# Kernel tuning notes

Measured on AMD Instinct MI355X. Metric: run time of the kernel, lower is better.

Reference implementation:

```python
import jax, jax.numpy as jnp
import numpy as np

B, T, D, H, L = 32, 1024, 512, 512, 2
FORGET_BIAS = 1.0


def setup_inputs() -> dict:
    key = jax.random.key(0)
    k_x, k_len, k_wf, k_wb = jax.random.split(key, 4)
    inputs = jax.random.normal(k_x, (B, T, D), dtype=jnp.float32)
    lengths = jax.random.randint(k_len, (B,), 1, T + 1, dtype=jnp.int32)
    scale = 1.0 / np.sqrt(D + H)
    # Stacked per-layer weights; layer input dim == H == D so shapes match.
    Wf = jax.random.normal(k_wf, (L, D + H, 4 * H), dtype=jnp.float32) * scale
    Wb = jax.random.normal(k_wb, (L, D + H, 4 * H), dtype=jnp.float32) * scale
    bf = jnp.zeros((L, 4 * H), dtype=jnp.float32)
    bb = jnp.zeros((L, 4 * H), dtype=jnp.float32)
    return {"inputs": inputs, "lengths": lengths, "Wf": Wf, "bf": bf, "Wb": Wb, "bb": bb}


def _reverse_sequence(x_bt, lengths):
    # TF reverse_sequence semantics: reverse the first `len` steps, keep the tail.
    t = jnp.arange(x_bt.shape[1])[None, :]                      # [1,T]
    ln = lengths[:, None]                                       # [B,1]
    idx = jnp.where(t < ln, ln - 1 - t, t)                      # [B,T]
    return jnp.take_along_axis(x_bt, idx[:, :, None], axis=1)


def _lstm_layer(xs_tb, W, b, lengths):
    # xs_tb: [T,B,In]; tf.contrib LSTMCell gate order: i, j(candidate), f, o.
    Bdim = xs_tb.shape[1]
    h0 = jnp.zeros((Bdim, H), xs_tb.dtype)
    c0 = jnp.zeros((Bdim, H), xs_tb.dtype)
    ts = jnp.arange(xs_tb.shape[0])

    def step(carry, inp):
        h, c = carry
        x, t = inp
        z = jnp.concatenate([x, h], axis=-1) @ W + b             # [B,4H]
        i, j, f, o = jnp.split(z, 4, axis=-1)
        c_new = jax.nn.sigmoid(f + FORGET_BIAS) * c + jax.nn.sigmoid(i) * jnp.tanh(j)
        h_new = jax.nn.sigmoid(o) * jnp.tanh(c_new)
        m = (t < lengths)[:, None]
        # dynamic_rnn: freeze state past length, emit zeros past length
        c_keep = jnp.where(m, c_new, c)
        h_keep = jnp.where(m, h_new, h)
        y = jnp.where(m, h_new, 0.0)
        return (h_keep, c_keep), y

    (hT, cT), ys = jax.lax.scan(step, (h0, c0), (xs_tb, ts))
    return ys, hT, cT


def reference(inputs, lengths, Wf, bf, Wb, bb):
    # Forward-direction stacked LSTM
    h = jnp.transpose(inputs, (1, 0, 2))                         # [T,B,D]
    for l in range(L):
        h, _, _ = _lstm_layer(h, Wf[l], bf[l], lengths)
    out_f = jnp.transpose(h, (1, 0, 2))                          # [B,T,H]

    # Backward direction: reverse by length, run stack, reverse back
    xr = _reverse_sequence(inputs, lengths)
    h = jnp.transpose(xr, (1, 0, 2))
    for l in range(L):
        h, _, _ = _lstm_layer(h, Wb[l], bb[l], lengths)
    out_b = _reverse_sequence(jnp.transpose(h, (1, 0, 2)), lengths)

    return jnp.concatenate([out_f, out_b], axis=2)               # [B,T,2H]
```

## Files before the change

kernel.cpp:

```cpp
#include <hip/hip_runtime.h>
#include <stdint.h>


#define B_ 32
#define T_ 1024
#define H_ 512

typedef __attribute__((ext_vector_type(8))) short bf16x8;
typedef __attribute__((ext_vector_type(4))) float f32x4;
typedef __attribute__((ext_vector_type(4))) unsigned int u32x4;
typedef unsigned long long ull;

#define FLAG_OFF  0
#define H_OFF     4096
#define H_GRP_U64 (2 * 8192)
#define R_OFF     (H_OFF + 4 * 2 * 65536)
#define R_DIR_U64 (8 * 4096)
#define WS_BYTES  (R_OFF + 2 * 8 * 32768)

#define BLO_OFF   0
#define BHI_OFF   65536
#define ZB0_OFF   131072
#define ZB1_OFF   (ZB0_OFF + 4224)
#define LDS_BYTES (ZB1_OFF + 4224)

#define LOADA(p)     __hip_atomic_load((p), __ATOMIC_RELAXED, __HIP_MEMORY_SCOPE_AGENT)
#define STOREA(p, v) __hip_atomic_store((p), (v), __ATOMIC_RELAXED, __HIP_MEMORY_SCOPE_AGENT)

__device__ __forceinline__ float sigm(float x) { return 1.f / (1.f + __expf(-x)); }
__device__ __forceinline__ unsigned short bf16_rtn(float f) {
  unsigned u = __builtin_bit_cast(unsigned, f);
  unsigned r = u + 0x7FFFu + ((u >> 16) & 1u);
  return (unsigned short)(r >> 16);
}
__device__ __forceinline__ float bf16f(unsigned short h) {
  return __builtin_bit_cast(float, (unsigned)h << 16);
}
__device__ __forceinline__ void split_f32(float f, unsigned short& hi, unsigned short& lo) {
  hi = bf16_rtn(f); lo = bf16_rtn(f - bf16f(hi));
}
__device__ __forceinline__ unsigned packhi2(float fa, float fb) {
  return __builtin_amdgcn_perm(__builtin_bit_cast(unsigned, fb),
                               __builtin_bit_cast(unsigned, fa), 0x07060302u);
}
__device__ __forceinline__ float hipart(float f) {
  return __builtin_bit_cast(float, __builtin_bit_cast(unsigned, f) & 0xFFFF0000u);
}
__device__ __forceinline__ unsigned hiPair(unsigned w0, unsigned w1) {
  return __builtin_amdgcn_perm(w1, w0, 0x07060302u);
}
__device__ __forceinline__ unsigned loPair(unsigned w0, unsigned w1) {
  return __builtin_amdgcn_perm(w1, w0, 0x05040100u);
}

#define MFMA(ACC, Af, Bf) ACC = __builtin_amdgcn_mfma_f32_16x16x32_bf16((Af), (Bf), (ACC), 0, 0, 0)

__global__ __launch_bounds__(256, 1)
void bilstm_v5(const float* __restrict__ inp, const int* __restrict__ lens,
               const float* __restrict__ Wf, const float* __restrict__ bfp,
               const float* __restrict__ Wb, const float* __restrict__ bbp,
               float* __restrict__ out, char* __restrict__ wsb) {
  extern __shared__ char lds[];
  const int tid = threadIdx.x, blk = blockIdx.x;
  const int xcd = blk & 7, slotp = blk >> 3;
  const int group = xcd >> 1;
  const int gslice = (xcd & 1) * 32 + slotp;
  const int j0 = gslice * 8;
  const int dir = group >> 1, layer = group & 1;

  unsigned* flags = (unsigned*)(wsb + FLAG_OFF) + dir * 128;
  ull*      hgq   = (ull*)(wsb + H_OFF) + (size_t)group * H_GRP_U64;
  unsigned* hgw   = (unsigned*)hgq;
  ull*      rgq   = (ull*)(wsb + R_OFF) + (size_t)dir * R_DIR_U64;
  unsigned* rgw   = (unsigned*)rgq;

  const float* Wg = (dir == 0 ? Wf : Wb) + (size_t)layer * 1024 * 2048;
  const float* bg = (dir == 0 ? bfp : bbp) + layer * 2048;

  for (int it = 0; it < 16; ++it) {
    int tt = tid + 256 * it;
    int k = tt >> 2, gate = tt & 3;
    const float* src = Wg + (size_t)k * 2048 + gate * 512 + j0;
    float4 w0 = *(const float4*)src, w1 = *(const float4*)(src + 4);
    float wv[8] = {w0.x, w0.y, w0.z, w0.w, w1.x, w1.y, w1.z, w1.w};
#pragma unroll
    for (int u = 0; u < 8; ++u) {
      int c = u * 4 + gate;
      unsigned short hi, lo; split_f32(wv[u], hi, lo);
      int byte = c * 2048 + ((k * 2) ^ ((c & 7) << 4));
      *(unsigned short*)(lds + BHI_OFF + byte) = hi;
      *(unsigned short*)(lds + BLO_OFF + byte) = lo;
    }
  }
  __syncthreads();

  const int lane = tid & 63, wvid = tid >> 6;
  const int bt = wvid >> 1, kq = wvid & 1;
  const int fr = lane & 15, fq = lane >> 4;

  bf16x8 bhX[2][8], bhH[2][8];
  int colN[2], xr[2];
#pragma unroll
  for (int nt = 0; nt < 2; ++nt) {
    colN[nt] = nt * 16 + fr;
    xr[nt] = (colN[nt] & 7) << 4;
    const char* base = lds + BHI_OFF + colN[nt] * 2048;
#pragma unroll
    for (int kk = 0; kk < 8; ++kk) {
      int off = (kq * 512 + kk * 64 + fq * 16) ^ xr[nt];
      bhX[nt][kk] = *(const bf16x8*)(base + off);
      bhH[nt][kk] = *(const bf16x8*)(base + 1024 + off);
    }
  }

  float* zb0 = (float*)(lds + ZB0_OFF);
  float* zb1 = (float*)(lds + ZB1_OFF);
  float* zbme = kq ? zb1 : zb0;

  const int bi = tid >> 3, jj = tid & 7;
  const int mylen = lens[bi];
  const int lenrow = lens[bt * 16 + fr];
  const float bias0 = bg[0 * 512 + j0 + jj];
  const float bias1 = bg[1 * 512 + j0 + jj];
  const float bias2 = bg[2 * 512 + j0 + jj];
  const float bias3 = bg[3 * 512 + j0 + jj];

  const int sbt = bi >> 4;
  const int fragp = j0 >> 5;
  const int lanep = ((j0 >> 3) & 3) * 16 + (bi & 15);
  const int hpos = ((sbt * 16 + fragp) * 64 + lanep) * 8 + jj;
  const int rpos = ((sbt * 16 + fragp) * 64 + lanep) * 4 + (jj >> 1);

  float c_reg = 0.f, h_reg = 0.f;

#pragma unroll 1
  for (int s = 0; s <= 1025; ++s) {
    const bool act = layer ? (s >= 2) : (s < 1024);
    const int t = layer ? (s - 2) : s;
    f32x4 a00 = {0,0,0,0}, a01 = {0,0,0,0}, a02 = {0,0,0,0};
    f32x4 a10 = {0,0,0,0}, a11 = {0,0,0,0}, a12 = {0,0,0,0};

    if (act) {
      if (layer == 0) {
        int tr = t;
        if (dir == 1) tr = (t < lenrow) ? (lenrow - 1 - t) : t;
        const float* xp = inp + ((size_t)(bt * 16 + fr) * T_ + tr) * 512 + kq * 256 + fq * 8;
#pragma unroll
        for (int kk = 0; kk < 8; ++kk) {
          float4 xa = *(const float4*)(xp + kk * 32);
          float4 xb = *(const float4*)(xp + kk * 32 + 4);
          unsigned h0 = packhi2(xa.x, xa.y), h1 = packhi2(xa.z, xa.w);
          unsigned h2 = packhi2(xb.x, xb.y), h3 = packhi2(xb.z, xb.w);
          unsigned l0 = packhi2(xa.x - hipart(xa.x), xa.y - hipart(xa.y));
          unsigned l1 = packhi2(xa.z - hipart(xa.z), xa.w - hipart(xa.w));
          unsigned l2 = packhi2(xb.x - hipart(xb.x), xb.y - hipart(xb.y));
          unsigned l3 = packhi2(xb.z - hipart(xb.z), xb.w - hipart(xb.w));
          u32x4 hv = {h0, h1, h2, h3}, lv = {l0, l1, l2, l3};
          bf16x8 ah = __builtin_bit_cast(bf16x8, hv);
          bf16x8 al = __builtin_bit_cast(bf16x8, lv);
          int ko = kq * 512 + kk * 64 + fq * 16;
          bf16x8 bl0 = *(const bf16x8*)(lds + BLO_OFF + colN[0] * 2048 + (ko ^ xr[0]));
          bf16x8 bl1 = *(const bf16x8*)(lds + BLO_OFF + colN[1] * 2048 + (ko ^ xr[1]));
          MFMA(a00, ah, bhX[0][kk]); MFMA(a01, ah, bl0); MFMA(a02, al, bhX[0][kk]);
          MFMA(a10, ah, bhX[1][kk]); MFMA(a11, ah, bl1); MFMA(a12, al, bhX[1][kk]);
        }
      } else {
        const ull* q = rgq + (size_t)(t & 7) * 4096 + bt * 2048 + kq * 1024 + lane * 2;
        ull rr[8][2];
#pragma unroll
        for (int kk = 0; kk < 8; ++kk) {
          rr[kk][0] = LOADA(q + kk * 128);
          rr[kk][1] = LOADA(q + kk * 128 + 1);
        }
#pragma unroll
        for (int kk = 0; kk < 8; ++kk) {
          bf16x8 ah = __builtin_bit_cast(bf16x8, rr[kk]);
          int ko = kq * 512 + kk * 64 + fq * 16;
          bf16x8 bl0 = *(const bf16x8*)(lds + BLO_OFF + colN[0] * 2048 + (ko ^ xr[0]));
          bf16x8 bl1 = *(const bf16x8*)(lds + BLO_OFF + colN[1] * 2048 + (ko ^ xr[1]));
          MFMA(a00, ah, bhX[0][kk]); MFMA(a01, ah, bl0);
          MFMA(a10, ah, bhX[1][kk]); MFMA(a11, ah, bl1);
        }
      }
    }

    if (wvid == 0) {
      const int tgt_own = s;
      const int tgt_oth = layer ? s : (s - 5);
      while (true) {
        int fa = (int)LOADA(flags + layer * 64 + lane);
        int fb = (int)LOADA(flags + (1 - layer) * 64 + lane);
        if (__all((fa >= tgt_own) && (fb >= tgt_oth))) break;
        __builtin_amdgcn_s_sleep(1);
      }
    }
    __syncthreads();
    asm volatile("" ::: "memory");

    if (act) {
      const ull* q = hgq + (size_t)(s & 1) * 8192 + bt * 4096 + kq * 2048 + lane * 4;
      ull ra[8][4];
#pragma unroll
      for (int kk = 0; kk < 8; ++kk) {
#pragma unroll
        for (int w = 0; w < 4; ++w) ra[kk][w] = LOADA(q + kk * 256 + w);
      }
#pragma unroll
      for (int kk = 0; kk < 8; ++kk) {
        unsigned w0 = (unsigned)ra[kk][0], w1 = (unsigned)(ra[kk][0] >> 32);
        unsigned w2 = (unsigned)ra[kk][1], w3 = (unsigned)(ra[kk][1] >> 32);
        unsigned w4 = (unsigned)ra[kk][2], w5 = (unsigned)(ra[kk][2] >> 32);
        unsigned w6 = (unsigned)ra[kk][3], w7 = (unsigned)(ra[kk][3] >> 32);
        u32x4 hv = {hiPair(w0, w1), hiPair(w2, w3), hiPair(w4, w5), hiPair(w6, w7)};
        u32x4 lv = {loPair(w0, w1), loPair(w2, w3), loPair(w4, w5), loPair(w6, w7)};
        bf16x8 ah = __builtin_bit_cast(bf16x8, hv);
        bf16x8 al = __builtin_bit_cast(bf16x8, lv);
        int ko = 1024 + kq * 512 + kk * 64 + fq * 16;
        bf16x8 bl0 = *(const bf16x8*)(lds + BLO_OFF + colN[0] * 2048 + (ko ^ xr[0]));
        bf16x8 bl1 = *(const bf16x8*)(lds + BLO_OFF + colN[1] * 2048 + (ko ^ xr[1]));
        MFMA(a00, ah, bhH[0][kk]); MFMA(a01, ah, bl0); MFMA(a02, al, bhH[0][kk]);
        MFMA(a10, ah, bhH[1][kk]); MFMA(a11, ah, bl1); MFMA(a12, al, bhH[1][kk]);
      }
      f32x4 v0 = a00 + a01 + a02, v1 = a10 + a11 + a12;
#pragma unroll
      for (int r = 0; r < 4; ++r) {
        zbme[(bt * 16 + fq * 4 + r) * 33 + fr] = v0[r];
        zbme[(bt * 16 + fq * 4 + r) * 33 + 16 + fr] = v1[r];
      }
    }
    __syncthreads();

    if (act) {
      const int zo = bi * 33 + jj * 4;
      float z0 = zb0[zo + 0] + zb1[zo + 0] + bias0;
      float z1 = zb0[zo + 1] + zb1[zo + 1] + bias1;
      float z2 = zb0[zo + 2] + zb1[zo + 2] + bias2;
      float z3 = zb0[zo + 3] + zb1[zo + 3] + bias3;
      float ig = sigm(z0), fg = sigm(z2 + 1.0f), og = sigm(z3);
      float cn = fg * c_reg + ig * tanhf(z1);
      float hn = og * tanhf(cn);
      const bool m = (t < mylen);
      if (m) { c_reg = cn; h_reg = hn; }
      unsigned short nh, nl; split_f32(h_reg, nh, nl);
      unsigned word = ((unsigned)nh << 16) | nl;
      STOREA(hgw + (size_t)((s + 1) & 1) * 16384 + hpos, word);
      if (layer == 0) {
        float y = m ? hn : 0.f;
        unsigned ry = bf16_rtn(y);
        unsigned nb = __shfl_down((int)ry, 1);
        if ((jj & 1) == 0)
          STOREA(rgw + (size_t)(t & 7) * 8192 + rpos, ry | (nb << 16));
      } else {
        int ot = t;
        if (dir == 1) ot = (t < mylen) ? (mylen - 1 - t) : t;
        out[((size_t)bi * T_ + ot) * 1024 + dir * 512 + j0 + jj] = m ? hn : 0.f;
      }
    }
    __syncthreads();
    if (tid == 0) STOREA(flags + layer * 64 + gslice, (unsigned)(s + 1));
  }
}

extern "C" void kernel_launch(void* const* d_in, const int* in_sizes, int n_in,
                              void* d_out, int out_size, void* d_ws, size_t ws_size,
                              hipStream_t stream) {
  const float* inp   = (const float*)d_in[0];
  const int*   lensp = (const int*)d_in[1];
  const float* Wf    = (const float*)d_in[2];
  const float* bfp   = (const float*)d_in[3];
  const float* Wb    = (const float*)d_in[4];
  const float* bbp   = (const float*)d_in[5];
  float*       outp  = (float*)d_out;
  char*        wsp   = (char*)d_ws;
  (void)in_sizes; (void)n_in; (void)out_size; (void)ws_size;

  hipMemsetAsync(d_ws, 0, WS_BYTES, stream);
  hipFuncSetAttribute((const void*)bilstm_v5,
                      hipFuncAttributeMaxDynamicSharedMemorySize, LDS_BYTES);
  bilstm_v5<<<dim3(256), dim3(256), LDS_BYTES, stream>>>(
      inp, lensp, Wf, bfp, Wb, bbp, outp, wsp);
}
```

Before: 7.327 ms.

## Split batch across blocks and warp-specialize input projection from recurrent step

Restructures the persistent BiLSTM kernel. Each direction/layer group is split by batch half, so each block owns 16 hidden units across 16 batch rows instead of 8 units across 32. Within a block, two waves precompute the input projection one step ahead (double-buffered in LDS) while the other two waves run the recurrent h-projection and the cell update. The single flag barrier is replaced by per-wave flags with bounded polling, and layer-0 outputs are forwarded through a global ring. The aim is to take the input GEMM and the output stores off the serial critical path. The cost is a bounded spin-wait of 4000 iterations that could silently proceed on a timeout, plus more complex cross-block ordering.

```diff
diff --git a/kernel.cpp b/kernel.cpp
--- a/kernel.cpp
+++ b/kernel.cpp
@@ -2,30 +2,30 @@
 #include <stdint.h>
 
 
-#define B_ 32
 #define T_ 1024
-#define H_ 512
 
 typedef __attribute__((ext_vector_type(8))) short bf16x8;
 typedef __attribute__((ext_vector_type(4))) float f32x4;
 typedef __attribute__((ext_vector_type(4))) unsigned int u32x4;
 typedef unsigned long long ull;
 
-#define FLAG_OFF  0
+#define HFLAG_OFF 0
+#define XFLAG_OFF 2048
 #define H_OFF     4096
-#define H_GRP_U64 (2 * 8192)
-#define R_OFF     (H_OFF + 4 * 2 * 65536)
-#define R_DIR_U64 (8 * 4096)
-#define WS_BYTES  (R_OFF + 2 * 8 * 32768)
+#define RING_OFF  (4096 + 8*2*32768)
+#define WS_BYTES  (RING_OFF + 4*8*16384)
+#define WS_ZERO   RING_OFF
 
 #define BLO_OFF   0
-#define BHI_OFF   65536
-#define ZB0_OFF   131072
-#define ZB1_OFF   (ZB0_OFF + 4224)
-#define LDS_BYTES (ZB1_OFF + 4224)
+#define TEMP_OFF  131072
+#define ZX_OFF    131072
+#define ZF_OFF    (ZX_OFF + 4*4352)
+#define SRING_OFF (ZF_OFF + 2*2304)
+#define SOUT_OFF  (SRING_OFF + 2*512)
+#define LDS_BYTES (SOUT_OFF + 2*1024)
 
 #define LOADA(p)     __hip_atomic_load((p), __ATOMIC_RELAXED, __HIP_MEMORY_SCOPE_AGENT)
-#define STOREA(p, v) __hip_atomic_store((p), (v), __ATOMIC_RELAXED, __HIP_MEMORY_SCOPE_AGENT)
+#define STOREA(p,v)  __hip_atomic_store((p), (v), __ATOMIC_RELAXED, __HIP_MEMORY_SCOPE_AGENT)
 
 __device__ __forceinline__ float sigm(float x) { return 1.f / (1.f + __expf(-x)); }
 __device__ __forceinline__ unsigned short bf16_rtn(float f) {
@@ -55,209 +55,280 @@
 
 #define MFMA(ACC, Af, Bf) ACC = __builtin_amdgcn_mfma_f32_16x16x32_bf16((Af), (Bf), (ACC), 0, 0, 0)
 
+__device__ __forceinline__ void poll64(const unsigned* p, unsigned tgt, int lane) {
+  for (int it = 0; it < 4000; ++it) {
+    unsigned v = LOADA(p + lane);
+    if (__all(v >= tgt)) return;
+    __builtin_amdgcn_s_sleep(2);
+  }
+}
+__device__ __forceinline__ void poll32(const unsigned* p, unsigned tgt, int lane) {
+  for (int it = 0; it < 4000; ++it) {
+    unsigned v = LOADA(p + (lane & 31));
+    if (__all(v >= tgt)) return;
+    __builtin_amdgcn_s_sleep(2);
+  }
+}
+
 __global__ __launch_bounds__(256, 1)
-void bilstm_v5(const float* __restrict__ inp, const int* __restrict__ lens,
+void bilstm_v9(const float* __restrict__ inp, const int* __restrict__ lens,
                const float* __restrict__ Wf, const float* __restrict__ bfp,
                const float* __restrict__ Wb, const float* __restrict__ bbp,
                float* __restrict__ out, char* __restrict__ wsb) {
   extern __shared__ char lds[];
   const int tid = threadIdx.x, blk = blockIdx.x;
-  const int xcd = blk & 7, slotp = blk >> 3;
-  const int group = xcd >> 1;
-  const int gslice = (xcd & 1) * 32 + slotp;
-  const int j0 = gslice * 8;
-  const int dir = group >> 1, layer = group & 1;
-
-  unsigned* flags = (unsigned*)(wsb + FLAG_OFF) + dir * 128;
-  ull*      hgq   = (ull*)(wsb + H_OFF) + (size_t)group * H_GRP_U64;
-  unsigned* hgw   = (unsigned*)hgq;
-  ull*      rgq   = (ull*)(wsb + R_OFF) + (size_t)dir * R_DIR_U64;
-  unsigned* rgw   = (unsigned*)rgq;
+  const int g = blk & 7, rank = blk >> 3;
+  const int dir = g >> 2, layer = (g >> 1) & 1, bhalf = g & 1;
+  const int j0 = rank * 16;
+
+  unsigned* hfl_own = (unsigned*)(wsb + HFLAG_OFF) + g * 64;
+  unsigned* xfl_own = (unsigned*)(wsb + XFLAG_OFF) + g * 64;
+  const unsigned* hfl_l1 = (const unsigned*)(wsb + HFLAG_OFF) + (g | 2) * 64;
+  const unsigned* xfl_l0 = (const unsigned*)(wsb + XFLAG_OFF) + (g & ~2) * 64;
+  unsigned* hbuf = (unsigned*)(wsb + H_OFF) + (size_t)g * 2 * 8192;
+  unsigned* ringbase = (unsigned*)(wsb + RING_OFF) + (size_t)(dir * 2 + bhalf) * 8 * 4096;
 
   const float* Wg = (dir == 0 ? Wf : Wb) + (size_t)layer * 1024 * 2048;
   const float* bg = (dir == 0 ? bfp : bbp) + layer * 2048;
 
-  for (int it = 0; it < 16; ++it) {
-    int tt = tid + 256 * it;
-    int k = tt >> 2, gate = tt & 3;
-    const float* src = Wg + (size_t)k * 2048 + gate * 512 + j0;
-    float4 w0 = *(const float4*)src, w1 = *(const float4*)(src + 4);
-    float wv[8] = {w0.x, w0.y, w0.z, w0.w, w1.x, w1.y, w1.z, w1.w};
-#pragma unroll
-    for (int u = 0; u < 8; ++u) {
-      int c = u * 4 + gate;
-      unsigned short hi, lo; split_f32(wv[u], hi, lo);
-      int byte = c * 2048 + ((k * 2) ^ ((c & 7) << 4));
-      *(unsigned short*)(lds + BHI_OFF + byte) = hi;
-      *(unsigned short*)(lds + BLO_OFF + byte) = lo;
-    }
+  const int lane = tid & 63, wvid = tid >> 6;
+  const bool isX = (wvid < 2);
+  const int hw = wvid - 2;
+  const int fr = lane & 15, fq = lane >> 4;
+  const int xsw = (fr & 7) << 4;
+
+  bf16x8 bhf[32];
+#pragma unroll 1
+  for (int c8 = 0; c8 < 8; ++c8) {
+#pragma unroll
+    for (int i = 0; i < 2; ++i) {
+      int task = tid * 2 + i;
+      int kl = task >> 2, gate = task & 3;
+      int kg = c8 * 128 + kl;
+      const float* src = Wg + (size_t)kg * 2048 + gate * 512 + j0;
+      float4 w0 = *(const float4*)src, w1 = *(const float4*)(src + 4);
+      float4 w2 = *(const float4*)(src + 8), w3 = *(const float4*)(src + 12);
+      float wv[16] = {w0.x, w0.y, w0.z, w0.w, w1.x, w1.y, w1.z, w1.w,
+                      w2.x, w2.y, w2.z, w2.w, w3.x, w3.y, w3.z, w3.w};
+#pragma unroll
+      for (int u = 0; u < 16; ++u) {
+        int cc = u * 4 + gate;
+        unsigned short hi, lo; split_f32(wv[u], hi, lo);
+        *(unsigned short*)(lds + TEMP_OFF + cc * 256 + kl * 2) = hi;
+        *(unsigned short*)(lds + BLO_OFF + cc * 2048 + ((kg * 2) ^ ((cc & 7) << 4))) = lo;
+      }
+    }
+    __syncthreads();
+    if (isX && (c8 >> 1) == wvid) {
+#pragma unroll
+      for (int kj = 0; kj < 4; ++kj) {
+        const int kk = (c8 & 1) * 4 + kj;
+        const int kl2 = (kk * 32 + fq * 8) * 2 - (c8 & 1) * 256;
+#pragma unroll
+        for (int nt = 0; nt < 4; ++nt)
+          bhf[nt * 8 + kk] = *(const bf16x8*)(lds + TEMP_OFF + (nt * 16 + fr) * 256 + kl2);
+      }
+    } else if (!isX && c8 >= 4) {
+#pragma unroll
+      for (int kj = 0; kj < 4; ++kj) {
+        const int kk = (c8 - 4) * 4 + kj;
+        const int kl2 = (kj * 32 + fq * 8) * 2;
+#pragma unroll
+        for (int nt = 0; nt < 2; ++nt)
+          bhf[nt * 16 + kk] = *(const bf16x8*)(lds + TEMP_OFF + (hw * 32 + nt * 16 + fr) * 256 + kl2);
+      }
+    }
+    __syncthreads();
   }
+
+  const int lenrow = lens[bhalf * 16 + fr];
+  const int lenx   = lens[bhalf * 16 + ((wvid * 64 + lane) >> 3)];
+  const int pb = lane & 15, pup = lane >> 4;
+  const int uloc = (isX ? 0 : hw * 8) + 2 * pup;
+  const int mylen = lens[bhalf * 16 + pb];
+  float bias_[2][4];
+#pragma unroll
+  for (int i = 0; i < 2; ++i)
+#pragma unroll
+    for (int g4 = 0; g4 < 4; ++g4)
+      bias_[i][g4] = bg[g4 * 512 + j0 + uloc + i];
+  float c_reg[2] = {0.f, 0.f}, h_reg[2] = {0.f, 0.f};
+  const int first_act = layer ? 4 : 0;
+
+  auto computeX0 = [&](int t, int par) {
+    f32x4 a[4][3] = {};
+    int tr = t;
+    if (dir == 1) tr = (t < lenrow) ? (lenrow - 1 - t) : t;
+    const float* xp = inp + ((size_t)(bhalf * 16 + fr) * T_ + tr) * 512 + wvid * 256 + fq * 8;
+#pragma unroll
+    for (int kk = 0; kk < 8; ++kk) {
+      float4 xa = *(const float4*)(xp + kk * 32);
+      float4 xb = *(const float4*)(xp + kk * 32 + 4);
+      unsigned h0 = packhi2(xa.x, xa.y), h1 = packhi2(xa.z, xa.w);
+      unsigned h2 = packhi2(xb.x, xb.y), h3 = packhi2(xb.z, xb.w);
+      unsigned l0 = packhi2(xa.x - hipart(xa.x), xa.y - hipart(xa.y));
+      unsigned l1 = packhi2(xa.z - hipart(xa.z), xa.w - hipart(xa.w));
+      unsigned l2 = packhi2(xb.x - hipart(xb.x), xb.y - hipart(xb.y));
+      unsigned l3 = packhi2(xb.z - hipart(xb.z), xb.w - hipart(xb.w));
+      u32x4 hv = {h0, h1, h2, h3}, lv = {l0, l1, l2, l3};
+      bf16x8 ah = __builtin_bit_cast(bf16x8, hv);
+      bf16x8 al = __builtin_bit_cast(bf16x8, lv);
+      const int ko = (wvid * 512 + kk * 64 + fq * 16) ^ xsw;
+#pragma unroll
+      for (int nt = 0; nt < 4; ++nt) {
+        bf16x8 bl = *(const bf16x8*)(lds + BLO_OFF + (nt * 16 + fr) * 2048 + ko);
+        MFMA(a[nt][0], ah, bhf[nt * 8 + kk]);
+        MFMA(a[nt][1], ah, bl);
+        MFMA(a[nt][2], al, bhf[nt * 8 + kk]);
+      }
+    }
+    float* zx = (float*)(lds + ZX_OFF) + (par * 2 + wvid) * 1088;
+#pragma unroll
+    for (int nt = 0; nt < 4; ++nt)
+#pragma unroll
+      for (int r = 0; r < 4; ++r)
+        zx[(fq * 4 + r) * 68 + nt * 16 + fr] = a[nt][0][r] + a[nt][1][r] + a[nt][2][r];
+  };
+
+  auto computeX1 = [&](int t, int par) {
+    poll32(xfl_l0, (unsigned)(t + 1), lane);
+    f32x4 a[4][2] = {};
+    const ull* q = (const ull*)(ringbase + (t & 7) * 4096 + fr * 256 + wvid * 128 + fq * 4);
+    ull rv[8][2];
+#pragma unroll
+    for (int kk = 0; kk < 8; ++kk) {
+      rv[kk][0] = LOADA(q + kk * 8);
+      rv[kk][1] = LOADA(q + kk * 8 + 1);
+    }
+#pragma unroll
+    for (int kk = 0; kk < 8; ++kk) {
+      bf16x8 ah = __builtin_bit_cast(bf16x8, rv[kk]);
+      const int ko = (wvid * 512 + kk * 64 + fq * 16) ^ xsw;
+#pragma unroll
+      for (int nt = 0; nt < 4; ++nt) {
+        bf16x8 bl = *(const bf16x8*)(lds + BLO_OFF + (nt * 16 + fr) * 2048 + ko);
+        MFMA(a[nt][0], ah, bhf[nt * 8 + kk]);
+        MFMA(a[nt][1], ah, bl);
+      }
+    }
+    float* zx = (float*)(lds + ZX_OFF) + (par * 2 + wvid) * 1088;
+#pragma unroll
+    for (int nt = 0; nt < 4; ++nt)
+#pragma unroll
+      for (int r = 0; r < 4; ++r)
+        zx[(fq * 4 + r) * 68 + nt * 16 + fr] = a[nt][0][r] + a[nt][1][r];
+  };
+
+  auto computeH = [&](int s) {
+    if (s > first_act) poll64(hfl_own, (unsigned)s, lane);
+    const ull* q = (const ull*)(hbuf + (size_t)(s & 1) * 8192) + fr * 256 + fq * 4;
+    f32x4 a[2][3] = {};
+    ull hr[4][4];
+#pragma unroll
+    for (int p = 0; p < 4; ++p)
+#pragma unroll
+      for (int w = 0; w < 4; ++w) hr[p][w] = LOADA(q + p * 16 + w);
+#pragma unroll
+    for (int kk = 0; kk < 16; ++kk) {
+      unsigned w0 = (unsigned)hr[kk & 3][0], w1 = (unsigned)(hr[kk & 3][0] >> 32);
+      unsigned w2 = (unsigned)hr[kk & 3][1], w3 = (unsigned)(hr[kk & 3][1] >> 32);
+      unsigned w4 = (unsigned)hr[kk & 3][2], w5 = (unsigned)(hr[kk & 3][2] >> 32);
+      unsigned w6 = (unsigned)hr[kk & 3][3], w7 = (unsigned)(hr[kk & 3][3] >> 32);
+      if (kk + 4 < 16) {
+#pragma unroll
+        for (int w = 0; w < 4; ++w) hr[kk & 3][w] = LOADA(q + (kk + 4) * 16 + w);
+      }
+      u32x4 hv = {hiPair(w0, w1), hiPair(w2, w3), hiPair(w4, w5), hiPair(w6, w7)};
+      u32x4 lv = {loPair(w0, w1), loPair(w2, w3), loPair(w4, w5), loPair(w6, w7)};
+      bf16x8 ah = __builtin_bit_cast(bf16x8, hv);
+      bf16x8 al = __builtin_bit_cast(bf16x8, lv);
+      const int ko = (1024 + kk * 64 + fq * 16) ^ xsw;
+#pragma unroll
+      for (int nt = 0; nt < 2; ++nt) {
+        bf16x8 bl = *(const bf16x8*)(lds + BLO_OFF + (hw * 32 + nt * 16 + fr) * 2048 + ko);
+        MFMA(a[nt][0], ah, bhf[nt * 16 + kk]);
+        MFMA(a[nt][1], ah, bl);
+        MFMA(a[nt][2], al, bhf[nt * 16 + kk]);
+      }
+    }
+    const float* zx0 = (const float*)(lds + ZX_OFF) + ((s & 1) * 2 + 0) * 1088;
+    const float* zx1 = (const float*)(lds + ZX_OFF) + ((s & 1) * 2 + 1) * 1088;
+    float* zf = (float*)(lds + ZF_OFF) + hw * 576;
+#pragma unroll
+    for (int nt = 0; nt < 2; ++nt) {
+      f32x4 v = a[nt][0] + a[nt][1] + a[nt][2];
+#pragma unroll
+      for (int r = 0; r < 4; ++r) {
+        const int row = fq * 4 + r, col = nt * 16 + fr;
+        zf[row * 36 + col] = v[r] + zx0[row * 68 + hw * 32 + col] + zx1[row * 68 + hw * 32 + col];
+      }
+    }
+    float4 z0 = *(const float4*)(zf + pb * 36 + 2 * pup * 4);
+    float4 z1 = *(const float4*)(zf + pb * 36 + 2 * pup * 4 + 4);
+    const int t = layer ? (s - 4) : s;
+    const bool m = (t < mylen);
+    float y[2];
+    unsigned hword[2];
+#pragma unroll
+    for (int i = 0; i < 2; ++i) {
+      float4 z = i ? z1 : z0;
+      float zi = z.x + bias_[i][0], zj = z.y + bias_[i][1];
+      float zfg = z.z + bias_[i][2], zo = z.w + bias_[i][3];
+      float ig = sigm(zi), fg = sigm(zfg + 1.0f), og = sigm(zo);
+      float cn = fg * c_reg[i] + ig * tanhf(zj);
+      float hn = og * tanhf(cn);
+      if (m) { c_reg[i] = cn; h_reg[i] = hn; }
+      unsigned short nh, nl; split_f32(h_reg[i], nh, nl);
+      hword[i] = ((unsigned)nh << 16) | nl;
+      y[i] = m ? hn : 0.f;
+    }
+    ull hq = (ull)hword[0] | ((ull)hword[1] << 32);
+    STOREA((ull*)(hbuf + (size_t)((s + 1) & 1) * 8192 + pb * 512 + j0 + uloc), hq);
+    if (layer == 0) {
+      unsigned rw = (unsigned)bf16_rtn(y[0]) | ((unsigned)bf16_rtn(y[1]) << 16);
+      *(unsigned*)(lds + SRING_OFF + (s & 1) * 512 + (pb * 8 + hw * 4 + pup) * 4) = rw;
+    } else {
+      *(float2*)(lds + SOUT_OFF + (s & 1) * 1024 + (pb * 8 + hw * 4 + pup) * 8) = make_float2(y[0], y[1]);
+    }
+    asm volatile("s_waitcnt vmcnt(0)" ::: "memory");
+    STOREA(hfl_own + rank * 2 + hw, (unsigned)(s + 1));
+  };
+
+  if (layer == 0 && isX) computeX0(0, 0);
   __syncthreads();
 
-  const int lane = tid & 63, wvid = tid >> 6;
-  const int bt = wvid >> 1, kq = wvid & 1;
-  const int fr = lane & 15, fq = lane >> 4;
-
-  bf16x8 bhX[2][8], bhH[2][8];
-  int colN[2], xr[2];
-#pragma unroll
-  for (int nt = 0; nt < 2; ++nt) {
-    colN[nt] = nt * 16 + fr;
-    xr[nt] = (colN[nt] & 7) << 4;
-    const char* base = lds + BHI_OFF + colN[nt] * 2048;
-#pragma unroll
-    for (int kk = 0; kk < 8; ++kk) {
-      int off = (kq * 512 + kk * 64 + fq * 16) ^ xr[nt];
-      bhX[nt][kk] = *(const bf16x8*)(base + off);
-      bhH[nt][kk] = *(const bf16x8*)(base + 1024 + off);
-    }
-  }
-
-  float* zb0 = (float*)(lds + ZB0_OFF);
-  float* zb1 = (float*)(lds + ZB1_OFF);
-  float* zbme = kq ? zb1 : zb0;
-
-  const int bi = tid >> 3, jj = tid & 7;
-  const int mylen = lens[bi];
-  const int lenrow = lens[bt * 16 + fr];
-  const float bias0 = bg[0 * 512 + j0 + jj];
-  const float bias1 = bg[1 * 512 + j0 + jj];
-  const float bias2 = bg[2 * 512 + j0 + jj];
-  const float bias3 = bg[3 * 512 + j0 + jj];
-
-  const int sbt = bi >> 4;
-  const int fragp = j0 >> 5;
-  const int lanep = ((j0 >> 3) & 3) * 16 + (bi & 15);
-  const int hpos = ((sbt * 16 + fragp) * 64 + lanep) * 8 + jj;
-  const int rpos = ((sbt * 16 + fragp) * 64 + lanep) * 4 + (jj >> 1);
-
-  float c_reg = 0.f, h_reg = 0.f;
-
 #pragma unroll 1
-  for (int s = 0; s <= 1025; ++s) {
-    const bool act = layer ? (s >= 2) : (s < 1024);
-    const int t = layer ? (s - 2) : s;
-    f32x4 a00 = {0,0,0,0}, a01 = {0,0,0,0}, a02 = {0,0,0,0};
-    f32x4 a10 = {0,0,0,0}, a11 = {0,0,0,0}, a12 = {0,0,0,0};
-
-    if (act) {
+  for (int s = 0; s <= 1028; ++s) {
+    if (isX) {
       if (layer == 0) {
-        int tr = t;
-        if (dir == 1) tr = (t < lenrow) ? (lenrow - 1 - t) : t;
-        const float* xp = inp + ((size_t)(bt * 16 + fr) * T_ + tr) * 512 + kq * 256 + fq * 8;
-#pragma unroll
-        for (int kk = 0; kk < 8; ++kk) {
-          float4 xa = *(const float4*)(xp + kk * 32);
-          float4 xb = *(const float4*)(xp + kk * 32 + 4);
-          unsigned h0 = packhi2(xa.x, xa.y), h1 = packhi2(xa.z, xa.w);
-          unsigned h2 = packhi2(xb.x, xb.y), h3 = packhi2(xb.z, xb.w);
-          unsigned l0 = packhi2(xa.x - hipart(xa.x), xa.y - hipart(xa.y));
-          unsigned l1 = packhi2(xa.z - hipart(xa.z), xa.w - hipart(xa.w));
-          unsigned l2 = packhi2(xb.x - hipart(xb.x), xb.y - hipart(xb.y));
-          unsigned l3 = packhi2(xb.z - hipart(xb.z), xb.w - hipart(xb.w));
-          u32x4 hv = {h0, h1, h2, h3}, lv = {l0, l1, l2, l3};
-          bf16x8 ah = __builtin_bit_cast(bf16x8, hv);
-          bf16x8 al = __builtin_bit_cast(bf16x8, lv);
-          int ko = kq * 512 + kk * 64 + fq * 16;
-          bf16x8 bl0 = *(const bf16x8*)(lds + BLO_OFF + colN[0] * 2048 + (ko ^ xr[0]));
-          bf16x8 bl1 = *(const bf16x8*)(lds + BLO_OFF + colN[1] * 2048 + (ko ^ xr[1]));
-          MFMA(a00, ah, bhX[0][kk]); MFMA(a01, ah, bl0); MFMA(a02, al, bhX[0][kk]);
-          MFMA(a10, ah, bhX[1][kk]); MFMA(a11, ah, bl1); MFMA(a12, al, bhX[1][kk]);
+        if (wvid == 0) {
+          const int tp = s - 1;
+          if (tp >= 0 && tp < 1024) {
+            if (s >= 9) poll64(hfl_l1, (unsigned)(s - 4), lane);
+            ull w = *(const ull*)(lds + SRING_OFF + (tp & 1) * 512 + lane * 8);
+            unsigned* dst = ringbase + (tp & 7) * 4096 + (lane >> 2) * 256 + rank * 8 + 2 * (lane & 3);
+            STOREA((ull*)dst, w);
+          }
+          asm volatile("s_waitcnt vmcnt(0)" ::: "memory");
+          STOREA(xfl_own + rank, (unsigned)s);
         }
+        if (s <= 1022) computeX0(s + 1, (s + 1) & 1);
       } else {
-        const ull* q = rgq + (size_t)(t & 7) * 4096 + bt * 2048 + kq * 1024 + lane * 2;
-        ull rr[8][2];
-#pragma unroll
-        for (int kk = 0; kk < 8; ++kk) {
-          rr[kk][0] = LOADA(q + kk * 128);
-          rr[kk][1] = LOADA(q + kk * 128 + 1);
+        const int tp = s - 5;
+        if (tp >= 0 && tp < 1024) {
+          const int i = wvid * 64 + lane, b = i >> 3, p = i & 7;
+          float2 yv = *(const float2*)(lds + SOUT_OFF + ((s - 1) & 1) * 1024 + (b * 8 + p) * 8);
+          const int bg2 = bhalf * 16 + b;
+          const int ot = (dir == 1 && tp < lenx) ? (lenx - 1 - tp) : tp;
+          *(float2*)(out + ((size_t)bg2 * T_ + ot) * 1024 + dir * 512 + j0 + 2 * p) = yv;
         }
-#pragma unroll
-        for (int kk = 0; kk < 8; ++kk) {
-          bf16x8 ah = __builtin_bit_cast(bf16x8, rr[kk]);
-          int ko = kq * 512 + kk * 64 + fq * 16;
-          bf16x8 bl0 = *(const bf16x8*)(lds + BLO_OFF + colN[0] * 2048 + (ko ^ xr[0]));
-          bf16x8 bl1 = *(const bf16x8*)(lds + BLO_OFF + colN[1] * 2048 + (ko ^ xr[1]));
-          MFMA(a00, ah, bhX[0][kk]); MFMA(a01, ah, bl0);
-          MFMA(a10, ah, bhX[1][kk]); MFMA(a11, ah, bl1);
-        }
-      }
-    }
-
-    if (wvid == 0) {
-      const int tgt_own = s;
-      const int tgt_oth = layer ? s : (s - 5);
-      while (true) {
-        int fa = (int)LOADA(flags + layer * 64 + lane);
-        int fb = (int)LOADA(flags + (1 - layer) * 64 + lane);
-        if (__all((fa >= tgt_own) && (fb >= tgt_oth))) break;
-        __builtin_amdgcn_s_sleep(1);
-      }
+        if (s >= 3 && s <= 1026) computeX1(s - 3, (s + 1) & 1);
+      }
+    } else {
+      const bool pa = layer ? (s >= 4 && s <= 1027) : (s <= 1023);
+      if (pa) computeH(s);
     }
     __syncthreads();
-    asm volatile("" ::: "memory");
-
-    if (act) {
-      const ull* q = hgq + (size_t)(s & 1) * 8192 + bt * 4096 + kq * 2048 + lane * 4;
-      ull ra[8][4];
-#pragma unroll
-      for (int kk = 0; kk < 8; ++kk) {
-#pragma unroll
-        for (int w = 0; w < 4; ++w) ra[kk][w] = LOADA(q + kk * 256 + w);
-      }
-#pragma unroll
-      for (int kk = 0; kk < 8; ++kk) {
-        unsigned w0 = (unsigned)ra[kk][0], w1 = (unsigned)(ra[kk][0] >> 32);
-        unsigned w2 = (unsigned)ra[kk][1], w3 = (unsigned)(ra[kk][1] >> 32);
-        unsigned w4 = (unsigned)ra[kk][2], w5 = (unsigned)(ra[kk][2] >> 32);
-        unsigned w6 = (unsigned)ra[kk][3], w7 = (unsigned)(ra[kk][3] >> 32);
-        u32x4 hv = {hiPair(w0, w1), hiPair(w2, w3), hiPair(w4, w5), hiPair(w6, w7)};
-        u32x4 lv = {loPair(w0, w1), loPair(w2, w3), loPair(w4, w5), loPair(w6, w7)};
-        bf16x8 ah = __builtin_bit_cast(bf16x8, hv);
-        bf16x8 al = __builtin_bit_cast(bf16x8, lv);
-        int ko = 1024 + kq * 512 + kk * 64 + fq * 16;
-        bf16x8 bl0 = *(const bf16x8*)(lds + BLO_OFF + colN[0] * 2048 + (ko ^ xr[0]));
-        bf16x8 bl1 = *(const bf16x8*)(lds + BLO_OFF + colN[1] * 2048 + (ko ^ xr[1]));
-        MFMA(a00, ah, bhH[0][kk]); MFMA(a01, ah, bl0); MFMA(a02, al, bhH[0][kk]);
-        MFMA(a10, ah, bhH[1][kk]); MFMA(a11, ah, bl1); MFMA(a12, al, bhH[1][kk]);
-      }
-      f32x4 v0 = a00 + a01 + a02, v1 = a10 + a11 + a12;
-#pragma unroll
-      for (int r = 0; r < 4; ++r) {
-        zbme[(bt * 16 + fq * 4 + r) * 33 + fr] = v0[r];
-        zbme[(bt * 16 + fq * 4 + r) * 33 + 16 + fr] = v1[r];
-      }
-    }
-    __syncthreads();
-
-    if (act) {
-      const int zo = bi * 33 + jj * 4;
-      float z0 = zb0[zo + 0] + zb1[zo + 0] + bias0;
-      float z1 = zb0[zo + 1] + zb1[zo + 1] + bias1;
-      float z2 = zb0[zo + 2] + zb1[zo + 2] + bias2;
-      float z3 = zb0[zo + 3] + zb1[zo + 3] + bias3;
-      float ig = sigm(z0), fg = sigm(z2 + 1.0f), og = sigm(z3);
-      float cn = fg * c_reg + ig * tanhf(z1);
-      float hn = og * tanhf(cn);
-      const bool m = (t < mylen);
-      if (m) { c_reg = cn; h_reg = hn; }
-      unsigned short nh, nl; split_f32(h_reg, nh, nl);
-      unsigned word = ((unsigned)nh << 16) | nl;
-      STOREA(hgw + (size_t)((s + 1) & 1) * 16384 + hpos, word);
-      if (layer == 0) {
-        float y = m ? hn : 0.f;
-        unsigned ry = bf16_rtn(y);
-        unsigned nb = __shfl_down((int)ry, 1);
-        if ((jj & 1) == 0)
-          STOREA(rgw + (size_t)(t & 7) * 8192 + rpos, ry | (nb << 16));
-      } else {
-        int ot = t;
-        if (dir == 1) ot = (t < mylen) ? (mylen - 1 - t) : t;
-        out[((size_t)bi * T_ + ot) * 1024 + dir * 512 + j0 + jj] = m ? hn : 0.f;
-      }
-    }
-    __syncthreads();
-    if (tid == 0) STOREA(flags + layer * 64 + gslice, (unsigned)(s + 1));
   }
 }
 
@@ -274,9 +345,9 @@
   char*        wsp   = (char*)d_ws;
   (void)in_sizes; (void)n_in; (void)out_size; (void)ws_size;
 
-  hipMemsetAsync(d_ws, 0, WS_BYTES, stream);
-  hipFuncSetAttribute((const void*)bilstm_v5,
+  hipMemsetAsync(d_ws, 0, WS_ZERO, stream);
+  hipFuncSetAttribute((const void*)bilstm_v9,
                       hipFuncAttributeMaxDynamicSharedMemorySize, LDS_BYTES);
-  bilstm_v5<<<dim3(256), dim3(256), LDS_BYTES, stream>>>(
+  bilstm_v9<<<dim3(256), dim3(256), LDS_BYTES, stream>>>(
       inp, lensp, Wf, bfp, Wb, bbp, outp, wsp);
 }
```

Result: slower. 11.11 ms (+51.6%).
